# Kernel optimization log

Hardware: AMD Instinct MI355X
Metric: run time of the kernel (lower is better)

The kernel has to match this reference:

```python
import jax, jax.numpy as jnp
import numpy as np

NEG_SLOPE = 0.2
MASK_FILL = -1e9


def setup_inputs() -> dict:
    key = jax.random.key(0)
    k1, k2, k3, k4 = jax.random.split(key, 4)
    B, N, IN_DIM = 4, 2048, 256
    H, D = 8, 64  # n_heads, hidden_dim (out_dim)
    nodes = jax.random.normal(k1, (B, N, IN_DIM), dtype=jnp.float32)
    edges = jax.random.randint(k2, (B, N, N), 0, 2, dtype=jnp.int32)
    # Xavier-uniform-ish init for params
    pw_lim = float(np.sqrt(6.0 / (IN_DIM + H * D)))
    proj_weights = jax.random.uniform(k3, (IN_DIM, H * D), dtype=jnp.float32,
                                      minval=-pw_lim, maxval=pw_lim)
    aw_lim = float(np.sqrt(6.0 / (H + 2 * D)))
    attn_weights = jax.random.uniform(k4, (H, 2 * D), dtype=jnp.float32,
                                      minval=-aw_lim, maxval=aw_lim)
    return {"nodes": nodes, "edges": edges,
            "proj_weights": proj_weights, "attn_weights": attn_weights}


def reference(nodes, edges, proj_weights, attn_weights):
    B, N, _ = nodes.shape
    H, twoD = attn_weights.shape
    D = twoD // 2
    # Projection: [B,N,in] @ [in,H*D] -> [B,H,N,D]
    mapped = jnp.matmul(nodes, proj_weights).reshape(B, N, H, D).transpose(0, 2, 1, 3)
    # The left@diag(a)@right^T trick is exactly a_l.h_i + a_r.h_j:
    a_l = attn_weights[:, :D]   # [H,D]
    a_r = attn_weights[:, D:]   # [H,D]
    el = jnp.einsum('bhnd,hd->bhn', mapped, a_l)  # score contribution of source i
    er = jnp.einsum('bhnd,hd->bhn', mapped, a_r)  # score contribution of target j
    scores = jax.nn.leaky_relu(el[:, :, :, None] + er[:, :, None, :],
                               negative_slope=NEG_SLOPE)  # [B,H,N,N]
    scores = jnp.where(edges[:, None, :, :] == 0, MASK_FILL, scores)
    attn = jax.nn.softmax(scores, axis=-1)  # dropout p=0 -> identity
    out = jnp.einsum('bhij,bhjd->bhid', attn, mapped)  # [B,H,N,D]
    out = out.transpose(0, 2, 1, 3).reshape(B, N, H * D)  # is_concat=True
    return jax.nn.sigmoid(out)
```

## Files before the change

kernel.cpp:

```cpp
#include <hip/hip_runtime.h>
#include <hip/hip_fp16.h>
#include <math.h>

#define NEG 0.2f
#define LOG2E 1.4426950408889634f

typedef float f32x4 __attribute__((ext_vector_type(4)));
typedef _Float16 half8 __attribute__((ext_vector_type(8)));
typedef _Float16 h2v __attribute__((ext_vector_type(2)));
typedef short s16x2 __attribute__((ext_vector_type(2)));

#if __has_builtin(__builtin_amdgcn_exp2f)
#define EXP2F(x) __builtin_amdgcn_exp2f(x)
#else
#define EXP2F(x) exp2f(x)
#endif

__device__ inline uint cvt2(float a, float b) {
  union {
    decltype(__builtin_amdgcn_cvt_pkrtz(0.f, 0.f)) v;
    uint u;
  } x;
  x.v = __builtin_amdgcn_cvt_pkrtz(a, b);
  return x.u;
}

__device__ inline h2v u2h(uint u) {
  union {
    uint u;
    h2v v;
  } x;
  x.u = u;
  return x.v;
}

__device__ inline uint h2u(h2v v) {
  union {
    uint u;
    h2v v;
  } x;
  x.v = v;
  return x.u;
}

__device__ inline uint sgn16(uint t) {
  union {
    uint u;
    s16x2 v;
  } x;
  x.u = t;
  x.v = x.v >> 15;
  return x.u;
}


__global__ __launch_bounds__(256, 4) void prep_pack(
    const float* __restrict__ W, ushort* __restrict__ wf, uint* __restrict__ ermx,
    const int* __restrict__ e, uint* __restrict__ epk32) {
  const int bx = blockIdx.x;
  const int t = threadIdx.x;
  const int l = t & 63;
  if (bx < 33) {
    if (bx == 32) {
      if (t < 32) ermx[t] = 0u;
      return;
    }
    const int h = bx >> 2, ct = bx & 3;
#pragma unroll
    for (int s = 0; s < 2; ++s) {
      int slot = t + s * 256;
      int ll = slot & 63, kk = slot >> 6;
      int col = h * 64 + ct * 16 + (ll & 15);
      int k0 = kk * 32 + (ll >> 4) * 8;
      uint outv[4];
#pragma unroll
      for (int c = 0; c < 4; ++c) {
        float x0 = W[(size_t)(k0 + 2 * c) * 512 + col];
        float x1 = W[(size_t)(k0 + 2 * c + 1) * 512 + col];
        outv[c] = cvt2(x0, x1);
      }
      *(uint4*)&wf[(((size_t)((h * 4 + ct) * 8 + kk)) * 64 + ll) * 8] = *(uint4*)outv;
    }
    return;
  }
  const size_t g0 = (size_t)(bx - 33) * 16 + (t >> 6) * 4;
#pragma unroll
  for (int it = 0; it < 4; ++it) {
    const size_t gi = g0 + it;
    int4 v = *(const int4*)(e + gi * 256 + l * 4);
    unsigned long long b0 = __ballot(v.x != 0);
    unsigned long long b1 = __ballot(v.y != 0);
    unsigned long long b2 = __ballot(v.z != 0);
    unsigned long long b3 = __ballot(v.w != 0);
    if (l == 0) {
      uint4 lo, hi;
      lo.x = (uint)b0;
      lo.y = (uint)b1;
      lo.z = (uint)b2;
      lo.w = (uint)b3;
      hi.x = (uint)(b0 >> 32);
      hi.y = (uint)(b1 >> 32);
      hi.z = (uint)(b2 >> 32);
      hi.w = (uint)(b3 >> 32);
      *(uint4*)&epk32[gi * 8] = lo;
      *(uint4*)&epk32[gi * 8 + 4] = hi;
    }
  }
}

__global__ __launch_bounds__(256, 4) void pack2_proj(
    const int* __restrict__ e, uint* __restrict__ epk32,
    const float* __restrict__ A, const ushort* __restrict__ wf,
    const float* __restrict__ aw, ushort* __restrict__ mt,
    float* __restrict__ el, float* __restrict__ er, uint* __restrict__ ermx) {
  __shared__ ushort ct_lds[64][72];
  const int bx = blockIdx.x;
  const int t = threadIdx.x;
  const int l = t & 63;
  if (bx % 3 != 2) {
    const int pb = (bx / 3) * 2 + (bx % 3);
    const size_t g0 = 32768 + (size_t)pb * 16 + (t >> 6) * 4;
#pragma unroll
    for (int it = 0; it < 4; ++it) {
      const size_t gi = g0 + it;
      int4 v = *(const int4*)(e + gi * 256 + l * 4);
      unsigned long long b0 = __ballot(v.x != 0);
      unsigned long long b1 = __ballot(v.y != 0);
      unsigned long long b2 = __ballot(v.z != 0);
      unsigned long long b3 = __ballot(v.w != 0);
      if (l == 0) {
        uint4 lo, hi;
        lo.x = (uint)b0;
        lo.y = (uint)b1;
        lo.z = (uint)b2;
        lo.w = (uint)b3;
        hi.x = (uint)(b0 >> 32);
        hi.y = (uint)(b1 >> 32);
        hi.z = (uint)(b2 >> 32);
        hi.w = (uint)(b3 >> 32);
        *(uint4*)&epk32[gi * 8] = lo;
        *(uint4*)&epk32[gi * 8 + 4] = hi;
      }
    }
    return;
  }
  const int pid = bx / 3;
  const int wq = t >> 6;
  const int i0 = (pid & 127) * 64;
  const int h = pid >> 7;
  const int b = i0 >> 11, n0 = i0 & 2047, bh = b * 8 + h;
  const int cl = l & 15, hi = l >> 4;
  const float* arow = A + (size_t)(i0 + wq * 16 + cl) * 256 + hi * 8;
  const int4* wfb = (const int4*)wf + (size_t)h * 32 * 64 + l;
  f32x4 acc[4];
#pragma unroll
  for (int ct = 0; ct < 4; ++ct) acc[ct] = (f32x4){0.f, 0.f, 0.f, 0.f};
#pragma unroll
  for (int kk = 0; kk < 8; ++kk) {
    float4 a0 = *(const float4*)(arow + kk * 32);
    float4 a1 = *(const float4*)(arow + kk * 32 + 4);
    union {
      uint u[4];
      half8 v;
    } af;
    af.u[0] = cvt2(a0.x, a0.y);
    af.u[1] = cvt2(a0.z, a0.w);
    af.u[2] = cvt2(a1.x, a1.y);
    af.u[3] = cvt2(a1.z, a1.w);
#pragma unroll
    for (int ct = 0; ct < 4; ++ct) {
      union {
        int4 i;
        half8 v;
      } bf;
      bf.i = wfb[((size_t)ct * 8 + kk) * 64];
      acc[ct] = __builtin_amdgcn_mfma_f32_16x16x32_f16(af.v, bf.v, acc[ct], 0, 0, 0);
    }
  }
  float alc[4], arc[4];
#pragma unroll
  for (int ct = 0; ct < 4; ++ct) {
    alc[ct] = aw[h * 128 + ct * 16 + cl];
    arc[ct] = aw[h * 128 + 64 + ct * 16 + cl];
  }
  float ermax_loc = -1e30f;
#pragma unroll
  for (int reg = 0; reg < 4; ++reg) {
    float pl = acc[0][reg] * alc[0] + acc[1][reg] * alc[1] + acc[2][reg] * alc[2] +
               acc[3][reg] * alc[3];
    float pr = acc[0][reg] * arc[0] + acc[1][reg] * arc[1] + acc[2][reg] * arc[2] +
               acc[3][reg] * arc[3];
#pragma unroll
    for (int s = 1; s < 16; s <<= 1) {
      pl += __shfl_xor(pl, s);
      pr += __shfl_xor(pr, s);
    }
    if (cl == 0) {
      int n = n0 + wq * 16 + hi * 4 + reg;
      el[(size_t)bh * 2048 + n] = pl;
      er[(size_t)bh * 2048 + n] = pr;
    }
    ermax_loc = fmaxf(ermax_loc, pr);
  }
  ermax_loc = fmaxf(ermax_loc, __shfl_xor(ermax_loc, 16));
  ermax_loc = fmaxf(ermax_loc, __shfl_xor(ermax_loc, 32));
  if (l == 0) {
    uint bits = __float_as_uint(ermax_loc);
    uint key = (bits & 0x80000000u) ? ~bits : (bits | 0x80000000u);
    atomicMax(&ermx[bh], key);
  }
#pragma unroll
  for (int ct = 0; ct < 4; ++ct) {
    ushort4 us;
    us.x = __half_as_ushort(__float2half(acc[ct][0]));
    us.y = __half_as_ushort(__float2half(acc[ct][1]));
    us.z = __half_as_ushort(__float2half(acc[ct][2]));
    us.w = __half_as_ushort(__float2half(acc[ct][3]));
    *(ushort4*)&ct_lds[ct * 16 + cl][wq * 16 + hi * 4] = us;
  }
  __syncthreads();
  {
    const int f = t >> 5, s = t & 31;
    const int g = f >> 2, nt = f & 3;
    const int r = nt * 16 + (s & 15);
    const int cm = g * 32 + (s >> 4) * 8;
    int4 v0 = *(const int4*)&ct_lds[r][cm];
    int4 v1 = *(const int4*)&ct_lds[r][cm + 16];
    const size_t base = ((size_t)bh * 32 + (n0 >> 6)) * 4096 + f * 512;
    *(int4*)&mt[base + s * 8] = v0;
    *(int4*)&mt[base + (s + 32) * 8] = v1;
  }
}

__global__ __launch_bounds__(256, 4) void gat_attn(
    const ushort* __restrict__ mt, const uint* __restrict__ epk32,
    const float* __restrict__ el, const float* __restrict__ er,
    const uint* __restrict__ ermx, float* __restrict__ out) {
  __shared__ __align__(16) char smem[24576];
  int4* vt4 = (int4*)smem;
  uint* ysh = (uint*)(smem + 16384);
  uint* vsh = (uint*)(smem + 20480);
  const int t = threadIdx.x;
  const int l = t & 63;
  const int wq = t >> 6;
  const int r16 = l & 15, hi = l >> 4;
  const int i0 = blockIdx.x * 64;
  const int h = blockIdx.y, b = blockIdx.z;
  const int bh = b * 8 + h;
  const uint ky = ermx[bh];
  const float emx = __uint_as_float((ky & 0x80000000u) ? (ky ^ 0x80000000u) : ~ky);
  {
    float4 e0 = *(const float4*)&er[(size_t)bh * 2048 + t * 8];
    float4 e1 = *(const float4*)&er[(size_t)bh * 2048 + t * 8 + 4];
    uint4 yp, vp;
    yp.x = cvt2(EXP2F((e0.x - emx) * LOG2E), EXP2F((e0.y - emx) * LOG2E));
    yp.y = cvt2(EXP2F((e0.z - emx) * LOG2E), EXP2F((e0.w - emx) * LOG2E));
    yp.z = cvt2(EXP2F((e1.x - emx) * LOG2E), EXP2F((e1.y - emx) * LOG2E));
    yp.w = cvt2(EXP2F((e1.z - emx) * LOG2E), EXP2F((e1.w - emx) * LOG2E));
    vp.x = cvt2(EXP2F((e0.x - emx) * (NEG * LOG2E)), EXP2F((e0.y - emx) * (NEG * LOG2E)));
    vp.y = cvt2(EXP2F((e0.z - emx) * (NEG * LOG2E)), EXP2F((e0.w - emx) * (NEG * LOG2E)));
    vp.z = cvt2(EXP2F((e1.x - emx) * (NEG * LOG2E)), EXP2F((e1.y - emx) * (NEG * LOG2E)));
    vp.w = cvt2(EXP2F((e1.z - emx) * (NEG * LOG2E)), EXP2F((e1.w - emx) * (NEG * LOG2E)));
    *(uint4*)&ysh[t * 4] = yp;
    *(uint4*)&vsh[t * 4] = vp;
  }
  const int irow = i0 + wq * 16 + r16;
  h2v X2, U2;
  {
    const float s0 = el[(size_t)bh * 2048 + irow] + emx;
    const float m2 = fmaxf(s0, NEG * s0) * LOG2E;
    const float Xf = EXP2F(s0 * LOG2E - m2);
    const float Uf = EXP2F(NEG * s0 * LOG2E - m2);
    X2 = u2h(cvt2(Xf, Xf));
    U2 = u2h(cvt2(Uf, Uf));
  }
  const uint* prow = epk32 + (size_t)(b * 2048 + irow) * 64;
  f32x4 acc[4];
  f32x4 accL = {0.f, 0.f, 0.f, 0.f};
#pragma unroll
  for (int nt = 0; nt < 4; ++nt) acc[nt] = (f32x4){0.f, 0.f, 0.f, 0.f};
  half8 ones;
#pragma unroll
  for (int c = 0; c < 8; ++c) ones[c] = (_Float16)1.f;

  const int4* srcbase = (const int4*)mt + (size_t)bh * 32 * 512 + wq * 128 + l;
  uint4 epw = *(const uint4*)&prow[0];
  {
    int4 p0 = srcbase[0];
    int4 p1 = srcbase[64];
    int4* d = vt4 + wq * 128 + l;
    d[0] = p0;
    d[64] = p1;
  }
  __syncthreads();
  int cur = 0;
  for (int jt = 0; jt < 32; ++jt) {
    int4 nx0, nx1;
    uint4 epwn;
    if (jt < 31) {
      const int4* s = srcbase + (size_t)(jt + 1) * 512;
      nx0 = s[0];
      nx1 = s[64];
      const int jn = jt + 1;
      epwn = *(const uint4*)&prow[((jn >> 2) << 3) + (((jn >> 1) & 1) << 2)];
    }
    half8 af[2];
#pragma unroll
    for (int g = 0; g < 2; ++g) {
      const uint idx = jt * 32 + g * 16 + hi * 4;
      uint4 y4 = *(const uint4*)&ysh[idx];
      uint4 v4 = *(const uint4*)&vsh[idx];
      const uint bsh = ((jt & 1) << 4) + (g << 3) + hi * 2;
      const uint p0 = epw.x >> bsh, p1 = epw.y >> bsh;
      const uint p2 = epw.z >> bsh, p3 = epw.w >> bsh;
      union {
        uint u[4];
        half8 v8;
      } fr;
      fr.u[0] = h2u(__builtin_elementwise_max(X2 * u2h(y4.x), U2 * u2h(v4.x))) &
                sgn16(((p0 & 1u) << 15) | (p1 << 31));
      fr.u[1] = h2u(__builtin_elementwise_max(X2 * u2h(y4.y), U2 * u2h(v4.y))) &
                sgn16(((p2 & 1u) << 15) | (p3 << 31));
      fr.u[2] = h2u(__builtin_elementwise_max(X2 * u2h(y4.z), U2 * u2h(v4.z))) &
                sgn16((((p0 >> 1) & 1u) << 15) | ((p1 >> 1) << 31));
      fr.u[3] = h2u(__builtin_elementwise_max(X2 * u2h(y4.w), U2 * u2h(v4.w))) &
                sgn16((((p2 >> 1) & 1u) << 15) | ((p3 >> 1) << 31));
      af[g] = fr.v8;
    }
    const half8* fb = (const half8*)(vt4 + cur * 512);
    __builtin_amdgcn_s_setprio(1);
#pragma unroll
    for (int g = 0; g < 2; ++g) {
      accL = __builtin_amdgcn_mfma_f32_16x16x32_f16(af[g], ones, accL, 0, 0, 0);
#pragma unroll
      for (int nt = 0; nt < 4; ++nt) {
        half8 bfr = fb[(g * 4 + nt) * 64 + l];
        acc[nt] = __builtin_amdgcn_mfma_f32_16x16x32_f16(af[g], bfr, acc[nt], 0, 0, 0);
      }
    }
    __builtin_amdgcn_s_setprio(0);
    if (jt < 31) {
      int4* d = vt4 + (cur ^ 1) * 512 + wq * 128 + l;
      d[0] = nx0;
      d[64] = nx1;
      epw = epwn;
    }
    __syncthreads();
    cur ^= 1;
  }
#pragma unroll
  for (int reg = 0; reg < 4; ++reg) {
    float invL = 1.f / accL[reg];
    int orow = i0 + wq * 16 + hi * 4 + reg;
#pragma unroll
    for (int nt = 0; nt < 4; ++nt) {
      float o = acc[nt][reg] * invL;
      float sig = 1.f / (1.f + __expf(-o));
      out[(size_t)(b * 2048 + orow) * 512 + h * 64 + nt * 16 + r16] = sig;
    }
  }
}

extern "C" void kernel_launch(void* const* d_in, const int* in_sizes, int n_in,
                              void* d_out, int out_size, void* d_ws, size_t ws_size,
                              hipStream_t stream) {
  const float* nodes = (const float*)d_in[0];
  const int* edges = (const int*)d_in[1];
  const float* pw = (const float*)d_in[2];
  const float* aw = (const float*)d_in[3];
  float* out = (float*)d_out;

  ushort* mt = (ushort*)d_ws;
  float* el = (float*)((char*)d_ws + 8388608);
  float* er = (float*)((char*)d_ws + 8650752);
  uint* ermx = (uint*)((char*)d_ws + 8912896);
  uint* epk = (uint*)((char*)d_ws + 8913024);
  ushort* wf = (ushort*)((char*)d_ws + 11010176);

  prep_pack<<<2081, 256, 0, stream>>>(pw, wf, ermx, edges, epk);
  pack2_proj<<<3072, 256, 0, stream>>>(edges, epk, nodes, wf, aw, mt, el, er, ermx);
  gat_attn<<<dim3(32, 8, 4), 256, 0, stream>>>(mt, epk, el, er, ermx, out);
}
```

Baseline: 87.40 us.

## Give each attention wave two 16-row tiles, halving waves per block

```diff
diff --git a/kernel.cpp b/kernel.cpp
--- a/kernel.cpp
+++ b/kernel.cpp
@@ -232,7 +232,7 @@
   }
 }
 
-__global__ __launch_bounds__(256, 4) void gat_attn(
+__global__ __launch_bounds__(128, 2) void gat_attn(
     const ushort* __restrict__ mt, const uint* __restrict__ epk32,
     const float* __restrict__ el, const float* __restrict__ er,
     const uint* __restrict__ ermx, float* __restrict__ out) {
@@ -250,113 +250,167 @@
   const uint ky = ermx[bh];
   const float emx = __uint_as_float((ky & 0x80000000u) ? (ky ^ 0x80000000u) : ~ky);
   {
-    float4 e0 = *(const float4*)&er[(size_t)bh * 2048 + t * 8];
-    float4 e1 = *(const float4*)&er[(size_t)bh * 2048 + t * 8 + 4];
-    uint4 yp, vp;
-    yp.x = cvt2(EXP2F((e0.x - emx) * LOG2E), EXP2F((e0.y - emx) * LOG2E));
-    yp.y = cvt2(EXP2F((e0.z - emx) * LOG2E), EXP2F((e0.w - emx) * LOG2E));
-    yp.z = cvt2(EXP2F((e1.x - emx) * LOG2E), EXP2F((e1.y - emx) * LOG2E));
-    yp.w = cvt2(EXP2F((e1.z - emx) * LOG2E), EXP2F((e1.w - emx) * LOG2E));
-    vp.x = cvt2(EXP2F((e0.x - emx) * (NEG * LOG2E)), EXP2F((e0.y - emx) * (NEG * LOG2E)));
-    vp.y = cvt2(EXP2F((e0.z - emx) * (NEG * LOG2E)), EXP2F((e0.w - emx) * (NEG * LOG2E)));
-    vp.z = cvt2(EXP2F((e1.x - emx) * (NEG * LOG2E)), EXP2F((e1.y - emx) * (NEG * LOG2E)));
-    vp.w = cvt2(EXP2F((e1.z - emx) * (NEG * LOG2E)), EXP2F((e1.w - emx) * (NEG * LOG2E)));
-    *(uint4*)&ysh[t * 4] = yp;
-    *(uint4*)&vsh[t * 4] = vp;
-  }
-  const int irow = i0 + wq * 16 + r16;
-  h2v X2, U2;
+#pragma unroll
+    for (int q = 0; q < 2; ++q) {
+      float4 e0 = *(const float4*)&er[(size_t)bh * 2048 + t * 16 + q * 8];
+      float4 e1 = *(const float4*)&er[(size_t)bh * 2048 + t * 16 + q * 8 + 4];
+      uint4 yp, vp;
+      yp.x = cvt2(EXP2F((e0.x - emx) * LOG2E), EXP2F((e0.y - emx) * LOG2E));
+      yp.y = cvt2(EXP2F((e0.z - emx) * LOG2E), EXP2F((e0.w - emx) * LOG2E));
+      yp.z = cvt2(EXP2F((e1.x - emx) * LOG2E), EXP2F((e1.y - emx) * LOG2E));
+      yp.w = cvt2(EXP2F((e1.z - emx) * LOG2E), EXP2F((e1.w - emx) * LOG2E));
+      vp.x = cvt2(EXP2F((e0.x - emx) * (NEG * LOG2E)), EXP2F((e0.y - emx) * (NEG * LOG2E)));
+      vp.y = cvt2(EXP2F((e0.z - emx) * (NEG * LOG2E)), EXP2F((e0.w - emx) * (NEG * LOG2E)));
+      vp.z = cvt2(EXP2F((e1.x - emx) * (NEG * LOG2E)), EXP2F((e1.y - emx) * (NEG * LOG2E)));
+      vp.w = cvt2(EXP2F((e1.z - emx) * (NEG * LOG2E)), EXP2F((e1.w - emx) * (NEG * LOG2E)));
+      *(uint4*)&ysh[t * 8 + q * 4] = yp;
+      *(uint4*)&vsh[t * 8 + q * 4] = vp;
+    }
+  }
+  const int irow0 = i0 + wq * 32 + r16;
+  const int irow1 = irow0 + 16;
+  h2v X2a, U2a, X2b, U2b;
   {
-    const float s0 = el[(size_t)bh * 2048 + irow] + emx;
-    const float m2 = fmaxf(s0, NEG * s0) * LOG2E;
-    const float Xf = EXP2F(s0 * LOG2E - m2);
-    const float Uf = EXP2F(NEG * s0 * LOG2E - m2);
-    X2 = u2h(cvt2(Xf, Xf));
-    U2 = u2h(cvt2(Uf, Uf));
-  }
-  const uint* prow = epk32 + (size_t)(b * 2048 + irow) * 64;
-  f32x4 acc[4];
-  f32x4 accL = {0.f, 0.f, 0.f, 0.f};
-#pragma unroll
-  for (int nt = 0; nt < 4; ++nt) acc[nt] = (f32x4){0.f, 0.f, 0.f, 0.f};
+    const float s0a = el[(size_t)bh * 2048 + irow0] + emx;
+    const float m2a = fmaxf(s0a, NEG * s0a) * LOG2E;
+    X2a = u2h(cvt2(EXP2F(s0a * LOG2E - m2a), EXP2F(s0a * LOG2E - m2a)));
+    U2a = u2h(cvt2(EXP2F(NEG * s0a * LOG2E - m2a), EXP2F(NEG * s0a * LOG2E - m2a)));
+    const float s0b = el[(size_t)bh * 2048 + irow1] + emx;
+    const float m2b = fmaxf(s0b, NEG * s0b) * LOG2E;
+    X2b = u2h(cvt2(EXP2F(s0b * LOG2E - m2b), EXP2F(s0b * LOG2E - m2b)));
+    U2b = u2h(cvt2(EXP2F(NEG * s0b * LOG2E - m2b), EXP2F(NEG * s0b * LOG2E - m2b)));
+  }
+  const uint* prow0 = epk32 + (size_t)(b * 2048 + irow0) * 64;
+  const uint* prow1 = prow0 + 1024;
+  f32x4 acc0[4], acc1[4];
+  f32x4 accL0 = {0.f, 0.f, 0.f, 0.f}, accL1 = {0.f, 0.f, 0.f, 0.f};
+#pragma unroll
+  for (int nt = 0; nt < 4; ++nt) {
+    acc0[nt] = (f32x4){0.f, 0.f, 0.f, 0.f};
+    acc1[nt] = (f32x4){0.f, 0.f, 0.f, 0.f};
+  }
   half8 ones;
 #pragma unroll
   for (int c = 0; c < 8; ++c) ones[c] = (_Float16)1.f;
 
-  const int4* srcbase = (const int4*)mt + (size_t)bh * 32 * 512 + wq * 128 + l;
-  uint4 epw = *(const uint4*)&prow[0];
+  const int4* srcbase = (const int4*)mt + (size_t)bh * 32 * 512 + t;
+  uint4 epw0 = *(const uint4*)&prow0[0];
+  uint4 epw1 = *(const uint4*)&prow1[0];
   {
     int4 p0 = srcbase[0];
-    int4 p1 = srcbase[64];
-    int4* d = vt4 + wq * 128 + l;
-    d[0] = p0;
-    d[64] = p1;
+    int4 p1 = srcbase[128];
+    int4 p2 = srcbase[256];
+    int4 p3 = srcbase[384];
+    vt4[t] = p0;
+    vt4[t + 128] = p1;
+    vt4[t + 256] = p2;
+    vt4[t + 384] = p3;
   }
   __syncthreads();
   int cur = 0;
   for (int jt = 0; jt < 32; ++jt) {
-    int4 nx0, nx1;
-    uint4 epwn;
+    int4 nx0, nx1, nx2, nx3;
+    uint4 epwn0, epwn1;
     if (jt < 31) {
       const int4* s = srcbase + (size_t)(jt + 1) * 512;
       nx0 = s[0];
-      nx1 = s[64];
+      nx1 = s[128];
+      nx2 = s[256];
+      nx3 = s[384];
       const int jn = jt + 1;
-      epwn = *(const uint4*)&prow[((jn >> 2) << 3) + (((jn >> 1) & 1) << 2)];
-    }
-    half8 af[2];
+      const int poff = ((jn >> 2) << 3) + (((jn >> 1) & 1) << 2);
+      epwn0 = *(const uint4*)&prow0[poff];
+      epwn1 = *(const uint4*)&prow1[poff];
+    }
+    half8 af0[2], af1[2];
 #pragma unroll
     for (int g = 0; g < 2; ++g) {
       const uint idx = jt * 32 + g * 16 + hi * 4;
       uint4 y4 = *(const uint4*)&ysh[idx];
       uint4 v4 = *(const uint4*)&vsh[idx];
       const uint bsh = ((jt & 1) << 4) + (g << 3) + hi * 2;
-      const uint p0 = epw.x >> bsh, p1 = epw.y >> bsh;
-      const uint p2 = epw.z >> bsh, p3 = epw.w >> bsh;
-      union {
-        uint u[4];
-        half8 v8;
-      } fr;
-      fr.u[0] = h2u(__builtin_elementwise_max(X2 * u2h(y4.x), U2 * u2h(v4.x))) &
-                sgn16(((p0 & 1u) << 15) | (p1 << 31));
-      fr.u[1] = h2u(__builtin_elementwise_max(X2 * u2h(y4.y), U2 * u2h(v4.y))) &
-                sgn16(((p2 & 1u) << 15) | (p3 << 31));
-      fr.u[2] = h2u(__builtin_elementwise_max(X2 * u2h(y4.z), U2 * u2h(v4.z))) &
-                sgn16((((p0 >> 1) & 1u) << 15) | ((p1 >> 1) << 31));
-      fr.u[3] = h2u(__builtin_elementwise_max(X2 * u2h(y4.w), U2 * u2h(v4.w))) &
-                sgn16((((p2 >> 1) & 1u) << 15) | ((p3 >> 1) << 31));
-      af[g] = fr.v8;
+      {
+        const uint p0 = epw0.x >> bsh, p1 = epw0.y >> bsh;
+        const uint p2 = epw0.z >> bsh, p3 = epw0.w >> bsh;
+        union {
+          uint u[4];
+          half8 v8;
+        } fr;
+        fr.u[0] = h2u(__builtin_elementwise_max(X2a * u2h(y4.x), U2a * u2h(v4.x))) &
+                  sgn16(((p0 & 1u) << 15) | (p1 << 31));
+        fr.u[1] = h2u(__builtin_elementwise_max(X2a * u2h(y4.y), U2a * u2h(v4.y))) &
+                  sgn16(((p2 & 1u) << 15) | (p3 << 31));
+        fr.u[2] = h2u(__builtin_elementwise_max(X2a * u2h(y4.z), U2a * u2h(v4.z))) &
+                  sgn16((((p0 >> 1) & 1u) << 15) | ((p1 >> 1) << 31));
+        fr.u[3] = h2u(__builtin_elementwise_max(X2a * u2h(y4.w), U2a * u2h(v4.w))) &
+                  sgn16((((p2 >> 1) & 1u) << 15) | ((p3 >> 1) << 31));
+        af0[g] = fr.v8;
+      }
+      {
+        const uint p0 = epw1.x >> bsh, p1 = epw1.y >> bsh;
+        const uint p2 = epw1.z >> bsh, p3 = epw1.w >> bsh;
+        union {
+          uint u[4];
+          half8 v8;
+        } fr;
+        fr.u[0] = h2u(__builtin_elementwise_max(X2b * u2h(y4.x), U2b * u2h(v4.x))) &
+                  sgn16(((p0 & 1u) << 15) | (p1 << 31));
+        fr.u[1] = h2u(__builtin_elementwise_max(X2b * u2h(y4.y), U2b * u2h(v4.y))) &
+                  sgn16(((p2 & 1u) << 15) | (p3 << 31));
+        fr.u[2] = h2u(__builtin_elementwise_max(X2b * u2h(y4.z), U2b * u2h(v4.z))) &
+                  sgn16((((p0 >> 1) & 1u) << 15) | ((p1 >> 1) << 31));
+        fr.u[3] = h2u(__builtin_elementwise_max(X2b * u2h(y4.w), U2b * u2h(v4.w))) &
+                  sgn16((((p2 >> 1) & 1u) << 15) | ((p3 >> 1) << 31));
+        af1[g] = fr.v8;
+      }
     }
     const half8* fb = (const half8*)(vt4 + cur * 512);
     __builtin_amdgcn_s_setprio(1);
 #pragma unroll
     for (int g = 0; g < 2; ++g) {
-      accL = __builtin_amdgcn_mfma_f32_16x16x32_f16(af[g], ones, accL, 0, 0, 0);
+      accL0 = __builtin_amdgcn_mfma_f32_16x16x32_f16(af0[g], ones, accL0, 0, 0, 0);
+      accL1 = __builtin_amdgcn_mfma_f32_16x16x32_f16(af1[g], ones, accL1, 0, 0, 0);
 #pragma unroll
       for (int nt = 0; nt < 4; ++nt) {
         half8 bfr = fb[(g * 4 + nt) * 64 + l];
-        acc[nt] = __builtin_amdgcn_mfma_f32_16x16x32_f16(af[g], bfr, acc[nt], 0, 0, 0);
+        acc0[nt] = __builtin_amdgcn_mfma_f32_16x16x32_f16(af0[g], bfr, acc0[nt], 0, 0, 0);
+        acc1[nt] = __builtin_amdgcn_mfma_f32_16x16x32_f16(af1[g], bfr, acc1[nt], 0, 0, 0);
       }
     }
     __builtin_amdgcn_s_setprio(0);
     if (jt < 31) {
-      int4* d = vt4 + (cur ^ 1) * 512 + wq * 128 + l;
-      d[0] = nx0;
-      d[64] = nx1;
-      epw = epwn;
+      int4* d = vt4 + (cur ^ 1) * 512;
+      d[t] = nx0;
+      d[t + 128] = nx1;
+      d[t + 256] = nx2;
+      d[t + 384] = nx3;
+      epw0 = epwn0;
+      epw1 = epwn1;
     }
     __syncthreads();
     cur ^= 1;
   }
 #pragma unroll
   for (int reg = 0; reg < 4; ++reg) {
-    float invL = 1.f / accL[reg];
-    int orow = i0 + wq * 16 + hi * 4 + reg;
-#pragma unroll
-    for (int nt = 0; nt < 4; ++nt) {
-      float o = acc[nt][reg] * invL;
-      float sig = 1.f / (1.f + __expf(-o));
-      out[(size_t)(b * 2048 + orow) * 512 + h * 64 + nt * 16 + r16] = sig;
+    {
+      float invL = 1.f / accL0[reg];
+      int orow = i0 + wq * 32 + hi * 4 + reg;
+#pragma unroll
+      for (int nt = 0; nt < 4; ++nt) {
+        float o = acc0[nt][reg] * invL;
+        float sig = 1.f / (1.f + __expf(-o));
+        out[(size_t)(b * 2048 + orow) * 512 + h * 64 + nt * 16 + r16] = sig;
+      }
+    }
+    {
+      float invL = 1.f / accL1[reg];
+      int orow = i0 + wq * 32 + 16 + hi * 4 + reg;
+#pragma unroll
+      for (int nt = 0; nt < 4; ++nt) {
+        float o = acc1[nt][reg] * invL;
+        float sig = 1.f / (1.f + __expf(-o));
+        out[(size_t)(b * 2048 + orow) * 512 + h * 64 + nt * 16 + r16] = sig;
+      }
     }
   }
 }
@@ -379,5 +433,5 @@
 
   prep_pack<<<2081, 256, 0, stream>>>(pw, wf, ermx, edges, epk);
   pack2_proj<<<3072, 256, 0, stream>>>(edges, epk, nodes, wf, aw, mt, el, er, ermx);
-  gat_attn<<<dim3(32, 8, 4), 256, 0, stream>>>(mt, epk, el, er, ermx, out);
-}
+  gat_attn<<<dim3(32, 8, 4), 128, 0, stream>>>(mt, epk, el, er, ermx, out);
+}
```

After: 95.28 us. +9.0%, slower.
